# Performance work log

Measured on AMD Instinct MI355X. Metric: run time of the kernel, lower is better.

## Reference

```python
import jax, jax.numpy as jnp
import numpy as np

N_LAYERS, HEADS, D_IN, D_OUT, T, D, DFF = 4, 8, 16, 3, 1024, 512, 2048
D_HEAD = D // HEADS


def sinusoidal_pos_enc(t, d):
    # Faithful to the source: base = pos / 10000**(emb_idx/d); sin on even cols, cos on odd cols
    pos = jnp.arange(t, dtype=jnp.float32)[:, None]
    emb = jnp.arange(d, dtype=jnp.float32)[None, :]
    base = pos / jnp.power(10000.0, emb / d)
    even = (jnp.arange(d) % 2 == 0)[None, :]
    return jnp.where(even, jnp.sin(base), jnp.cos(base))  # (t, d)


def layer_norm(x, g, b, eps=1e-5):
    m = x.mean(-1, keepdims=True)
    v = ((x - m) ** 2).mean(-1, keepdims=True)
    return (x - m) / jnp.sqrt(v + eps) * g + b


def setup_inputs() -> dict:
    key = jax.random.key(0)
    ks = iter(jax.random.split(key, 24))
    s = 0.02
    inp = {}
    inp['x'] = jax.random.normal(next(ks), (16, T, D_IN), dtype=jnp.float32)
    inp['pad_mask'] = jax.random.randint(next(ks), (16, T), 0, 2, dtype=jnp.int32)
    inp['enc_W'] = jax.random.normal(next(ks), (D_IN, D), dtype=jnp.float32) * s
    inp['enc_b'] = jnp.zeros((D,), jnp.float32)
    for name in ['Wq', 'Wk', 'Wv', 'Wo']:
        inp[name] = jax.random.normal(next(ks), (N_LAYERS, D, D), dtype=jnp.float32) * s
    inp['ff_W1'] = jax.random.normal(next(ks), (N_LAYERS, D, DFF), dtype=jnp.float32) * s
    inp['ff_b1'] = jnp.zeros((N_LAYERS, DFF), jnp.float32)
    inp['ff_W2'] = jax.random.normal(next(ks), (N_LAYERS, DFF, D), dtype=jnp.float32) * s
    inp['ff_b2'] = jnp.zeros((N_LAYERS, D), jnp.float32)
    inp['ln1_g'] = jnp.ones((N_LAYERS, D), jnp.float32)
    inp['ln1_b'] = jnp.zeros((N_LAYERS, D), jnp.float32)
    inp['ln2_g'] = jnp.ones((N_LAYERS, D), jnp.float32)
    inp['ln2_b'] = jnp.zeros((N_LAYERS, D), jnp.float32)
    inp['out_W'] = jax.random.normal(next(ks), (D * T, D_OUT), dtype=jnp.float32) * s
    inp['out_b'] = jnp.zeros((D_OUT,), jnp.float32)
    return inp


def reference(x, enc_W, enc_b, Wq, Wk, Wv, Wo, ff_W1, ff_b1, ff_W2, ff_b2,
              ln1_g, ln1_b, ln2_g, ln2_b, out_W, out_b, pad_mask):
    n, t = x.shape[0], x.shape[1]
    # InputEncoding (linear) scaled by sqrt(d_model)
    h = (x @ enc_W + enc_b) * jnp.sqrt(jnp.float32(D))
    # Sinusoidal positional encoding, zeroed at masked (pad_mask==0) timesteps
    pe = sinusoidal_pos_enc(t, D)[None]  # (1, t, d)
    pe = jnp.where(pad_mask[..., None] == 0, 0.0, pe)  # (n, t, d)
    h = h + pe
    mask4 = (pad_mask[..., None, None] == 0)  # (n, t, 1, 1)
    for i in range(N_LAYERS):
        # --- MultiHeadAttention (faithful to source's transpose quirk) ---
        Qh = (h @ Wq[i]).reshape(n, t, HEADS, D_HEAD).swapaxes(2, 3)  # (n,t,dh,H)
        Kh = (h @ Wk[i]).reshape(n, t, HEADS, D_HEAD)                 # (n,t,H,dh)
        Vh = (h @ Wv[i]).reshape(n, t, HEADS, D_HEAD).swapaxes(2, 3)  # (n,t,dh,H)
        # energy: per-timestep (dh x dh), scaled by d_head**1/2 == d_head/2 (source precedence)
        energy = jnp.matmul(Qh, Kh) / (D_HEAD / 2.0)                  # (n,t,dh,dh)
        energy = jnp.where(mask4, -1e20, energy)
        attn = jax.nn.softmax(energy, axis=-1)
        head = jnp.matmul(attn, Vh)                                   # (n,t,dh,H)
        out = head.reshape(n, t, D) @ Wo[i]
        # residual + layer norm
        h = layer_norm(out + h, ln1_g[i], ln1_b[i])
        # --- FFN (relu) ---
        ff = jax.nn.relu(h @ ff_W1[i] + ff_b1[i]) @ ff_W2[i] + ff_b2[i]
        h = layer_norm(ff + h, ln2_g[i], ln2_b[i])
    # mode='train': flatten and project
    return h.reshape(n, -1) @ out_W + out_b  # (n, d_output)
```

## Files before the change

### kernel.cpp

```cpp
#include <hip/hip_runtime.h>
#include <cmath>

#define NB 16
#define TSEQ 1024
#define DIN 16
#define DM 512
#define DFFN 2048
#define NLAYERS 4
#define DOUTN 3
#define ROWS (NB*TSEQ)

typedef unsigned short u16;
typedef short bf16x8 __attribute__((ext_vector_type(8)));
typedef u16   u16x4  __attribute__((ext_vector_type(4)));
typedef float f32x4  __attribute__((ext_vector_type(4)));

__device__ __forceinline__ float b2f(u16 v) { return __uint_as_float((unsigned)v << 16); }
__device__ __forceinline__ u16 f2b(float f) {
    unsigned u = __float_as_uint(f);
    return (u16)((u + 0x7FFFu + ((u >> 16) & 1u)) >> 16);
}

#define GLL(gp, lp) __builtin_amdgcn_global_load_lds( \
    (const __attribute__((address_space(1))) unsigned int*)(gp), \
    (__attribute__((address_space(3))) unsigned int*)(lp), 16, 0, 0)

__global__ __launch_bounds__(256) void transpose_cast(
    const float* __restrict__ in, u16* __restrict__ out,
    int K, int N, size_t in_lstride, size_t out_lstride)
{
    in  += (size_t)blockIdx.z * in_lstride;
    out += (size_t)blockIdx.z * out_lstride;
    __shared__ float t[32][33];
    int bk = blockIdx.x * 32, bn = blockIdx.y * 32;
    int x = threadIdx.x & 31, y = threadIdx.x >> 5;
    #pragma unroll
    for (int i = 0; i < 32; i += 8)
        t[y + i][x] = in[(size_t)(bk + y + i) * N + bn + x];
    __syncthreads();
    #pragma unroll
    for (int i = 0; i < 32; i += 8)
        out[(size_t)(bn + y + i) * K + bk + x] = f2b(t[x][y + i]);
}

__global__ __launch_bounds__(128) void encode_kernel(
    const float* __restrict__ x, const int* __restrict__ pad,
    const float* __restrict__ W, const float* __restrict__ b,
    u16* __restrict__ h)
{
    int row = blockIdx.x;
    int t   = row & (TSEQ - 1);
    int c   = threadIdx.x * 4;
    float acc[4];
    #pragma unroll
    for (int j = 0; j < 4; ++j) acc[j] = b[c + j];
    const float* xr = x + (size_t)row * DIN;
    #pragma unroll
    for (int k = 0; k < DIN; ++k) {
        float xv = xr[k];
        const float* wr = W + (size_t)k * DM + c;
        #pragma unroll
        for (int j = 0; j < 4; ++j) acc[j] += xv * wr[j];
    }
    const float s = 22.62741699796952f;
    bool has_pe = (pad[row] != 0);
    u16x4 o;
    #pragma unroll
    for (int j = 0; j < 4; ++j) {
        acc[j] *= s;
        if (has_pe) {
            int d = c + j;
            float base = (float)t * powf(10000.0f, -(float)d * (1.0f/512.0f));
            acc[j] += ((d & 1) == 0) ? sinf(base) : cosf(base);
        }
        o[j] = f2b(acc[j]);
    }
    *(u16x4*)&h[(size_t)row * DM + c] = o;
}

template<int BIAS, int RELU>
__global__ __launch_bounds__(256) void gemm_bf16(
    const u16* __restrict__ A, const u16* __restrict__ Bt,
    const float* __restrict__ bias, u16* __restrict__ C,
    int M, int N, int K)
{
    __shared__ u16 As[128 * 64];
    __shared__ u16 Bs[128 * 64];
    const int tid  = threadIdx.x;
    const int lane = tid & 63;
    const int wid  = tid >> 6;
    const int wr   = wid >> 1, wc = wid & 1;
    const int bm   = blockIdx.x * 128;
    const int bn   = blockIdx.y * 128;

    const int srow8 = lane >> 3;
    const int sslot = lane & 7;
    const int scol  = ((sslot ^ srow8) * 8);
    const u16* Ag = A  + (size_t)(bm + wid * 32 + srow8) * K + scol;
    const u16* Bg = Bt + (size_t)(bn + wid * 32 + srow8) * K + scol;
    u16* Al = As + wid * 2048;
    u16* Bl = Bs + wid * 2048;

    f32x4 acc[4][4];
    #pragma unroll
    for (int m = 0; m < 4; ++m)
        #pragma unroll
        for (int n = 0; n < 4; ++n)
            acc[m][n] = (f32x4){0.f, 0.f, 0.f, 0.f};

    const int fr  = lane & 15;
    const int grp = lane >> 4;

    for (int k0 = 0; k0 < K; k0 += 64) {
        #pragma unroll
        for (int i = 0; i < 4; ++i) {
            GLL(Ag + (size_t)(i * 8) * K + k0, Al + i * 512);
            GLL(Bg + (size_t)(i * 8) * K + k0, Bl + i * 512);
        }
        __syncthreads();
        bf16x8 a[4][2];
        #pragma unroll
        for (int m = 0; m < 4; ++m) {
            int row = wr * 64 + m * 16 + fr;
            #pragma unroll
            for (int ks = 0; ks < 2; ++ks) {
                int slot = (ks * 4 + grp) ^ (row & 7);
                a[m][ks] = *(const bf16x8*)(As + row * 64 + slot * 8);
            }
        }
        #pragma unroll
        for (int n = 0; n < 4; ++n) {
            bf16x8 b[2];
            int row = wc * 64 + n * 16 + fr;
            #pragma unroll
            for (int ks = 0; ks < 2; ++ks) {
                int slot = (ks * 4 + grp) ^ (row & 7);
                b[ks] = *(const bf16x8*)(Bs + row * 64 + slot * 8);
            }
            #pragma unroll
            for (int m = 0; m < 4; ++m) {
                acc[m][n] = __builtin_amdgcn_mfma_f32_16x16x32_bf16(a[m][0], b[0], acc[m][n], 0, 0, 0);
                acc[m][n] = __builtin_amdgcn_mfma_f32_16x16x32_bf16(a[m][1], b[1], acc[m][n], 0, 0, 0);
            }
        }
        __syncthreads();
    }

    float bb[4] = {0.f, 0.f, 0.f, 0.f};
    if (BIAS) {
        #pragma unroll
        for (int n = 0; n < 4; ++n) bb[n] = bias[bn + wc * 64 + n * 16 + fr];
    }
    #pragma unroll
    for (int m = 0; m < 4; ++m) {
        #pragma unroll
        for (int n = 0; n < 4; ++n) {
            int col = bn + wc * 64 + n * 16 + fr;
            #pragma unroll
            for (int j = 0; j < 4; ++j) {
                int row = bm + wr * 64 + m * 16 + ((lane >> 4) << 2) + j;
                float v = acc[m][n][j];
                if (BIAS) v += bb[n];
                if (RELU) v = fmaxf(v, 0.f);
                C[(size_t)row * N + col] = f2b(v);
            }
        }
    }
}

__global__ __launch_bounds__(256) void attn_mfma(
    const u16* __restrict__ QKV, const int* __restrict__ pad,
    u16* __restrict__ O)
{
    constexpr int WLDS = 6208;
    __shared__ u16 sh[4 * WLDS];
    const int wid  = threadIdx.x >> 6;
    const int lane = threadIdx.x & 63;
    const int site = blockIdx.x * 4 + wid;
    u16* Ql = sh + wid * WLDS;
    u16* Kl = Ql + 512;
    u16* Vl = Ql + 1024;
    u16* P  = Ql + 1600;
    u16* Ol = Ql + 5696;

    const u16* base = QKV + (size_t)site * 1536;
    *(bf16x8*)(Ql + lane * 8) = *(const bf16x8*)(base + lane * 8);
    *(bf16x8*)(Kl + lane * 8) = *(const bf16x8*)(base + 512 + lane * 8);
    {
        bf16x8 v = *(const bf16x8*)(base + 1024 + lane * 8);
        *(bf16x8*)(Vl + (lane >> 3) * 72 + (lane & 7) * 8) = v;
    }

    const int fr  = lane & 15;
    const int grp = lane >> 4;
    const bool masked = (pad[site] == 0);
    const bf16x8 zb = {0,0,0,0,0,0,0,0};
    const f32x4  zf = {0.f,0.f,0.f,0.f};

    if (masked) {
        const u16 c = f2b(1.0f / 64.0f);
        bf16x8 cv = {(short)c,(short)c,(short)c,(short)c,(short)c,(short)c,(short)c,(short)c};
        #pragma unroll
        for (int i = 0; i < 8; ++i)
            *(bf16x8*)(P + i * 512 + lane * 8) = cv;
    } else {
        bf16x8 aq[4], bk[4];
        #pragma unroll
        for (int m = 0; m < 4; ++m) { aq[m] = zb; bk[m] = zb; }
        if (grp == 0) {
            #pragma unroll
            for (int m = 0; m < 4; ++m)
                #pragma unroll
                for (int j = 0; j < 8; ++j) {
                    aq[m][j] = (short)Ql[j * 64 + m * 16 + fr];
                    bk[m][j] = (short)Kl[j * 64 + m * 16 + fr];
                }
        }
        #pragma unroll
        for (int m = 0; m < 4; ++m) {
            f32x4 ev[4];
            #pragma unroll
            for (int n = 0; n < 4; ++n)
                ev[n] = __builtin_amdgcn_mfma_f32_16x16x32_bf16(aq[m], bk[n], zf, 0, 0, 0);
            #pragma unroll
            for (int j = 0; j < 4; ++j) {
                float v = fmaxf(fmaxf(ev[0][j], ev[1][j]), fmaxf(ev[2][j], ev[3][j]));
                v = fmaxf(v, __shfl_xor(v, 1));
                v = fmaxf(v, __shfl_xor(v, 2));
                v = fmaxf(v, __shfl_xor(v, 4));
                v = fmaxf(v, __shfl_xor(v, 8));
                float p0 = __expf((ev[0][j] - v) * 0.03125f);
                float p1 = __expf((ev[1][j] - v) * 0.03125f);
                float p2 = __expf((ev[2][j] - v) * 0.03125f);
                float p3 = __expf((ev[3][j] - v) * 0.03125f);
                float s = p0 + p1 + p2 + p3;
                s += __shfl_xor(s, 1);
                s += __shfl_xor(s, 2);
                s += __shfl_xor(s, 4);
                s += __shfl_xor(s, 8);
                float inv = 1.0f / s;
                int row = m * 16 + grp * 4 + j;
                int sw  = (row & 7) << 3;
                P[(row * 64 +  0 + fr) ^ sw] = f2b(p0 * inv);
                P[(row * 64 + 16 + fr) ^ sw] = f2b(p1 * inv);
                P[(row * 64 + 32 + fr) ^ sw] = f2b(p2 * inv);
                P[(row * 64 + 48 + fr) ^ sw] = f2b(p3 * inv);
            }
        }
    }

    bf16x8 bv[2];
    #pragma unroll
    for (int ks = 0; ks < 2; ++ks) {
        int kb = ks * 32 + grp * 8;
        bv[ks] = (fr < 8) ? *(const bf16x8*)(Vl + fr * 72 + kb) : zb;
    }
    f32x4 pv[4];
    #pragma unroll
    for (int m = 0; m < 4; ++m) pv[m] = zf;
    #pragma unroll
    for (int m = 0; m < 4; ++m) {
        #pragma unroll
        for (int ks = 0; ks < 2; ++ks) {
            int row = m * 16 + fr;
            int off = (row * 64 + ks * 32 + grp * 8) ^ ((row & 7) << 3);
            bf16x8 ap = *(const bf16x8*)(P + off);
            pv[m] = __builtin_amdgcn_mfma_f32_16x16x32_bf16(ap, bv[ks], pv[m], 0, 0, 0);
        }
    }
    #pragma unroll
    for (int m = 0; m < 4; ++m)
        #pragma unroll
        for (int j = 0; j < 4; ++j) {
            int row = m * 16 + grp * 4 + j;
            if (fr < 8) Ol[row * 8 + fr] = f2b(pv[m][j]);
        }
    bf16x8 o = *(const bf16x8*)(Ol + lane * 8);
    *(bf16x8*)(O + (size_t)site * DM + lane * 8) = o;
}

__global__ __launch_bounds__(256) void add_ln_kernel(
    const u16* __restrict__ A, u16* __restrict__ H,
    const float* __restrict__ g, const float* __restrict__ b)
{
    int row  = blockIdx.x * 4 + (threadIdx.x >> 6);
    int lane = threadIdx.x & 63;
    const u16* a = A + (size_t)row * DM + lane * 8;
    u16* h = H + (size_t)row * DM + lane * 8;
    bf16x8 av = *(const bf16x8*)a;
    bf16x8 hv = *(const bf16x8*)h;
    float v[8];
    float s = 0.f;
    #pragma unroll
    for (int j = 0; j < 8; ++j) { v[j] = b2f((u16)av[j]) + b2f((u16)hv[j]); s += v[j]; }
    #pragma unroll
    for (int off = 32; off > 0; off >>= 1) s += __shfl_xor(s, off, 64);
    float mean = s * (1.0f / 512.0f);
    float var = 0.f;
    #pragma unroll
    for (int j = 0; j < 8; ++j) { float d = v[j] - mean; var += d * d; }
    #pragma unroll
    for (int off = 32; off > 0; off >>= 1) var += __shfl_xor(var, off, 64);
    float rstd = rsqrtf(var * (1.0f / 512.0f) + 1e-5f);
    bf16x8 ov;
    #pragma unroll
    for (int j = 0; j < 8; ++j) {
        int d = lane * 8 + j;
        ov[j] = (short)f2b((v[j] - mean) * rstd * g[d] + b[d]);
    }
    *(bf16x8*)h = ov;
}

__global__ __launch_bounds__(256) void out_stage1(
    const u16* __restrict__ h, const float* __restrict__ W,
    float* __restrict__ partial)
{
    int b = blockIdx.x, s = blockIdx.y;
    int tid = threadIdx.x;
    const u16* hb = h + (size_t)b * (TSEQ * DM) + (size_t)s * 8192;
    const float* Wb = W + (size_t)s * 8192 * 3;
    float a0 = 0.f, a1 = 0.f, a2 = 0.f;
    #pragma unroll 4
    for (int it = 0; it < 32; ++it) {
        int i = it * 256 + tid;
        float hv = b2f(hb[i]);
        a0 += hv * Wb[i * 3 + 0];
        a1 += hv * Wb[i * 3 + 1];
        a2 += hv * Wb[i * 3 + 2];
    }
    __shared__ float red[3][256];
    red[0][tid] = a0; red[1][tid] = a1; red[2][tid] = a2;
    __syncthreads();
    for (int off = 128; off > 0; off >>= 1) {
        if (tid < off) {
            red[0][tid] += red[0][tid + off];
            red[1][tid] += red[1][tid + off];
            red[2][tid] += red[2][tid + off];
        }
        __syncthreads();
    }
    if (tid == 0) {
        partial[(b * 64 + s) * 3 + 0] = red[0][0];
        partial[(b * 64 + s) * 3 + 1] = red[1][0];
        partial[(b * 64 + s) * 3 + 2] = red[2][0];
    }
}

__global__ __launch_bounds__(64) void out_stage2(
    const float* __restrict__ partial, const float* __restrict__ ob,
    float* __restrict__ out)
{
    int t = threadIdx.x;
    if (t < NB * DOUTN) {
        int b = t / 3, o = t % 3;
        float s = ob[o];
        for (int k = 0; k < 64; ++k) s += partial[(b * 64 + k) * 3 + o];
        out[t] = s;
    }
}

extern "C" void kernel_launch(void* const* d_in, const int* in_sizes, int n_in,
                              void* d_out, int out_size, void* d_ws, size_t ws_size,
                              hipStream_t stream)
{
    const float* x    = (const float*)d_in[0];
    const int*   pad  = (const int*)  d_in[1];
    const float* encW = (const float*)d_in[2];
    const float* encB = (const float*)d_in[3];
    const float* Wq   = (const float*)d_in[4];
    const float* Wk   = (const float*)d_in[5];
    const float* Wv   = (const float*)d_in[6];
    const float* Wo   = (const float*)d_in[7];
    const float* fW1  = (const float*)d_in[8];
    const float* fb1  = (const float*)d_in[9];
    const float* fW2  = (const float*)d_in[10];
    const float* fb2  = (const float*)d_in[11];
    const float* l1g  = (const float*)d_in[12];
    const float* l1b  = (const float*)d_in[13];
    const float* l2g  = (const float*)d_in[14];
    const float* l2b  = (const float*)d_in[15];
    const float* outW = (const float*)d_in[16];
    const float* outB = (const float*)d_in[17];
    float* out = (float*)d_out;

    const size_t WL  = 3145728;
    const size_t BUF = (size_t)ROWS * DM;
    const size_t need = (4 * WL + 6 * BUF) * sizeof(u16);
    if (ws_size < need) return;
    u16* wt = (u16*)d_ws;
    u16* h  = wt + 4 * WL;
    u16* b0 = h  + BUF;
    u16* b3 = b0 + 3 * BUF;
    u16* b4 = b3 + BUF;

    transpose_cast<<<dim3(16,16,4), 256, 0, stream>>>(Wq,  wt + 0,       512,  512,  (size_t)512*512,  WL);
    transpose_cast<<<dim3(16,16,4), 256, 0, stream>>>(Wk,  wt + 262144,  512,  512,  (size_t)512*512,  WL);
    transpose_cast<<<dim3(16,16,4), 256, 0, stream>>>(Wv,  wt + 524288,  512,  512,  (size_t)512*512,  WL);
    transpose_cast<<<dim3(16,16,4), 256, 0, stream>>>(Wo,  wt + 786432,  512,  512,  (size_t)512*512,  WL);
    transpose_cast<<<dim3(16,64,4), 256, 0, stream>>>(fW1, wt + 1048576, 512,  2048, (size_t)512*2048, WL);
    transpose_cast<<<dim3(64,16,4), 256, 0, stream>>>(fW2, wt + 2097152, 2048, 512,  (size_t)2048*512, WL);

    encode_kernel<<<ROWS, 128, 0, stream>>>(x, pad, encW, encB, h);

    for (int l = 0; l < NLAYERS; ++l) {
        u16* wl = wt + (size_t)l * WL;
        gemm_bf16<0,0><<<dim3(128,12), 256, 0, stream>>>(h, wl, nullptr, b0, ROWS, 1536, DM);
        attn_mfma<<<ROWS/4, 256, 0, stream>>>(b0, pad, b3);
        gemm_bf16<0,0><<<dim3(128,4), 256, 0, stream>>>(b3, wl + 786432, nullptr, b4, ROWS, DM, DM);
        add_ln_kernel<<<ROWS/4, 256, 0, stream>>>(b4, h, l1g + l*DM, l1b + l*DM);
        gemm_bf16<1,1><<<dim3(128,16), 256, 0, stream>>>(h, wl + 1048576, fb1 + (size_t)l*DFFN, b0, ROWS, DFFN, DM);
        gemm_bf16<1,0><<<dim3(128,4),  256, 0, stream>>>(b0, wl + 2097152, fb2 + (size_t)l*DM, b4, ROWS, DM, DFFN);
        add_ln_kernel<<<ROWS/4, 256, 0, stream>>>(b4, h, l2g + l*DM, l2b + l*DM);
    }

    out_stage1<<<dim3(NB, 64), 256, 0, stream>>>(h, outW, (float*)b0);
    out_stage2<<<1, 64, 0, stream>>>((float*)b0, outB, out);
}
```

Baseline: 852.8 us.

## Permute Q/K columns in QKV GEMM epilogue and shrink attention LDS footprint

The QKV GEMM epilogue now writes the Q and K columns in a transposed head-interleaved order, so the attention kernel can load its MFMA operands directly from global memory instead of staging Q, K and V through LDS with scalar gathers. Masked sites skip the softmax and the P·V MFMA and instead write the per-head mean of V directly. The attention P matrix is stored in two halves through a smaller swizzled LDS buffer, with the second half kept in registers until the first half has been consumed. This cuts per-wave LDS from about 12 KB to 5 KB, which raises occupancy, at the cost of scattered 2-byte stores in the QKV epilogue.

```diff
diff --git a/kernel.cpp b/kernel.cpp
--- a/kernel.cpp
+++ b/kernel.cpp
@@ -11,6 +11,7 @@
 #define ROWS (NB*TSEQ)
 
 typedef unsigned short u16;
+typedef unsigned int   u32;
 typedef short bf16x8 __attribute__((ext_vector_type(8)));
 typedef u16   u16x4  __attribute__((ext_vector_type(4)));
 typedef float f32x4  __attribute__((ext_vector_type(4)));
@@ -78,7 +79,7 @@
     *(u16x4*)&h[(size_t)row * DM + c] = o;
 }
 
-template<int BIAS, int RELU>
+template<int BIAS, int RELU, int QKPERM>
 __global__ __launch_bounds__(256) void gemm_bf16(
     const u16* __restrict__ A, const u16* __restrict__ Bt,
     const float* __restrict__ bias, u16* __restrict__ C,
@@ -156,13 +157,18 @@
         #pragma unroll
         for (int n = 0; n < 4; ++n) {
             int col = bn + wc * 64 + n * 16 + fr;
+            int colw = col;
+            if (QKPERM) {
+                if (col < 1024)
+                    colw = (col & 512) | (((col & 63) << 3) | ((col >> 6) & 7));
+            }
             #pragma unroll
             for (int j = 0; j < 4; ++j) {
                 int row = bm + wr * 64 + m * 16 + ((lane >> 4) << 2) + j;
                 float v = acc[m][n][j];
                 if (BIAS) v += bb[n];
                 if (RELU) v = fmaxf(v, 0.f);
-                C[(size_t)row * N + col] = f2b(v);
+                C[(size_t)row * N + colw] = f2b(v);
             }
         }
     }
@@ -172,102 +178,105 @@
     const u16* __restrict__ QKV, const int* __restrict__ pad,
     u16* __restrict__ O)
 {
-    constexpr int WLDS = 6208;
+    constexpr int WLDS = 2560;
     __shared__ u16 sh[4 * WLDS];
     const int wid  = threadIdx.x >> 6;
     const int lane = threadIdx.x & 63;
     const int site = blockIdx.x * 4 + wid;
-    u16* Ql = sh + wid * WLDS;
-    u16* Kl = Ql + 512;
-    u16* Vl = Ql + 1024;
-    u16* P  = Ql + 1600;
-    u16* Ol = Ql + 5696;
+    u16* P2 = sh + wid * WLDS;
+    u16* Ol = P2 + 2048;
 
     const u16* base = QKV + (size_t)site * 1536;
-    *(bf16x8*)(Ql + lane * 8) = *(const bf16x8*)(base + lane * 8);
-    *(bf16x8*)(Kl + lane * 8) = *(const bf16x8*)(base + 512 + lane * 8);
-    {
-        bf16x8 v = *(const bf16x8*)(base + 1024 + lane * 8);
-        *(bf16x8*)(Vl + (lane >> 3) * 72 + (lane & 7) * 8) = v;
-    }
-
     const int fr  = lane & 15;
     const int grp = lane >> 4;
-    const bool masked = (pad[site] == 0);
     const bf16x8 zb = {0,0,0,0,0,0,0,0};
     const f32x4  zf = {0.f,0.f,0.f,0.f};
 
-    if (masked) {
-        const u16 c = f2b(1.0f / 64.0f);
-        bf16x8 cv = {(short)c,(short)c,(short)c,(short)c,(short)c,(short)c,(short)c,(short)c};
-        #pragma unroll
-        for (int i = 0; i < 8; ++i)
-            *(bf16x8*)(P + i * 512 + lane * 8) = cv;
-    } else {
-        bf16x8 aq[4], bk[4];
-        #pragma unroll
-        for (int m = 0; m < 4; ++m) { aq[m] = zb; bk[m] = zb; }
-        if (grp == 0) {
-            #pragma unroll
-            for (int m = 0; m < 4; ++m)
-                #pragma unroll
-                for (int j = 0; j < 8; ++j) {
-                    aq[m][j] = (short)Ql[j * 64 + m * 16 + fr];
-                    bk[m][j] = (short)Kl[j * 64 + m * 16 + fr];
-                }
-        }
-        #pragma unroll
-        for (int m = 0; m < 4; ++m) {
-            f32x4 ev[4];
-            #pragma unroll
-            for (int n = 0; n < 4; ++n)
-                ev[n] = __builtin_amdgcn_mfma_f32_16x16x32_bf16(aq[m], bk[n], zf, 0, 0, 0);
-            #pragma unroll
-            for (int j = 0; j < 4; ++j) {
-                float v = fmaxf(fmaxf(ev[0][j], ev[1][j]), fmaxf(ev[2][j], ev[3][j]));
-                v = fmaxf(v, __shfl_xor(v, 1));
-                v = fmaxf(v, __shfl_xor(v, 2));
-                v = fmaxf(v, __shfl_xor(v, 4));
-                v = fmaxf(v, __shfl_xor(v, 8));
-                float p0 = __expf((ev[0][j] - v) * 0.03125f);
-                float p1 = __expf((ev[1][j] - v) * 0.03125f);
-                float p2 = __expf((ev[2][j] - v) * 0.03125f);
-                float p3 = __expf((ev[3][j] - v) * 0.03125f);
-                float s = p0 + p1 + p2 + p3;
-                s += __shfl_xor(s, 1);
-                s += __shfl_xor(s, 2);
-                s += __shfl_xor(s, 4);
-                s += __shfl_xor(s, 8);
-                float inv = 1.0f / s;
-                int row = m * 16 + grp * 4 + j;
-                int sw  = (row & 7) << 3;
-                P[(row * 64 +  0 + fr) ^ sw] = f2b(p0 * inv);
-                P[(row * 64 + 16 + fr) ^ sw] = f2b(p1 * inv);
-                P[(row * 64 + 32 + fr) ^ sw] = f2b(p2 * inv);
-                P[(row * 64 + 48 + fr) ^ sw] = f2b(p3 * inv);
-            }
-        }
-    }
-
+    if (pad[site] == 0) {
+        bf16x8 vv = *(const bf16x8*)(base + 1024 + lane * 8);
+        float s = 0.f;
+        #pragma unroll
+        for (int j = 0; j < 8; ++j) s += b2f((u16)vv[j]);
+        s += __shfl_xor(s, 1); s += __shfl_xor(s, 2); s += __shfl_xor(s, 4);
+        s *= (1.0f / 64.0f);
+        bf16x8 ov;
+        #pragma unroll
+        for (int h2 = 0; h2 < 8; ++h2) ov[h2] = (short)f2b(__shfl(s, h2 * 8));
+        *(bf16x8*)(O + (size_t)site * DM + lane * 8) = ov;
+        return;
+    }
+
+    bf16x8 bk[4];
+    #pragma unroll
+    for (int n = 0; n < 4; ++n)
+        bk[n] = (grp == 0) ? *(const bf16x8*)(base + 512 + (n * 16 + fr) * 8) : zb;
     bf16x8 bv[2];
     #pragma unroll
-    for (int ks = 0; ks < 2; ++ks) {
-        int kb = ks * 32 + grp * 8;
-        bv[ks] = (fr < 8) ? *(const bf16x8*)(Vl + fr * 72 + kb) : zb;
-    }
+    for (int ks = 0; ks < 2; ++ks)
+        bv[ks] = (fr < 8) ? *(const bf16x8*)(base + 1024 + fr * 64 + ks * 32 + grp * 8) : zb;
+
+    u32 p23[16];
+    #pragma unroll
+    for (int m = 0; m < 4; ++m) {
+        bf16x8 aq = (grp == 0) ? *(const bf16x8*)(base + (m * 16 + fr) * 8) : zb;
+        f32x4 ev[4];
+        #pragma unroll
+        for (int n = 0; n < 4; ++n)
+            ev[n] = __builtin_amdgcn_mfma_f32_16x16x32_bf16(aq, bk[n], zf, 0, 0, 0);
+        #pragma unroll
+        for (int j = 0; j < 4; ++j) {
+            float v = fmaxf(fmaxf(ev[0][j], ev[1][j]), fmaxf(ev[2][j], ev[3][j]));
+            v = fmaxf(v, __shfl_xor(v, 1));
+            v = fmaxf(v, __shfl_xor(v, 2));
+            v = fmaxf(v, __shfl_xor(v, 4));
+            v = fmaxf(v, __shfl_xor(v, 8));
+            float p0 = __expf((ev[0][j] - v) * 0.03125f);
+            float p1 = __expf((ev[1][j] - v) * 0.03125f);
+            float p2 = __expf((ev[2][j] - v) * 0.03125f);
+            float p3 = __expf((ev[3][j] - v) * 0.03125f);
+            float s = p0 + p1 + p2 + p3;
+            s += __shfl_xor(s, 1);
+            s += __shfl_xor(s, 2);
+            s += __shfl_xor(s, 4);
+            s += __shfl_xor(s, 8);
+            float inv = 1.0f / s;
+            int r  = m * 16 + grp * 4 + j;
+            int sw = j ^ grp;
+            P2[r * 32 + (((fr >> 3) ^ sw) * 8) + (fr & 7)]       = f2b(p0 * inv);
+            P2[r * 32 + (((2 + (fr >> 3)) ^ sw) * 8) + (fr & 7)] = f2b(p1 * inv);
+            p23[m * 4 + j] = (u32)f2b(p2 * inv) | ((u32)f2b(p3 * inv) << 16);
+        }
+    }
+
     f32x4 pv[4];
     #pragma unroll
-    for (int m = 0; m < 4; ++m) pv[m] = zf;
-    #pragma unroll
     for (int m = 0; m < 4; ++m) {
-        #pragma unroll
-        for (int ks = 0; ks < 2; ++ks) {
-            int row = m * 16 + fr;
-            int off = (row * 64 + ks * 32 + grp * 8) ^ ((row & 7) << 3);
-            bf16x8 ap = *(const bf16x8*)(P + off);
-            pv[m] = __builtin_amdgcn_mfma_f32_16x16x32_bf16(ap, bv[ks], pv[m], 0, 0, 0);
-        }
-    }
+        int row = m * 16 + fr;
+        int slot = grp ^ (fr & 3) ^ (fr >> 2);
+        bf16x8 ap = *(const bf16x8*)(P2 + row * 32 + slot * 8);
+        pv[m] = __builtin_amdgcn_mfma_f32_16x16x32_bf16(ap, bv[0], zf, 0, 0, 0);
+    }
+    asm volatile("s_waitcnt lgkmcnt(0)" ::: "memory");
+    __builtin_amdgcn_sched_barrier(0);
+
+    #pragma unroll
+    for (int m = 0; m < 4; ++m)
+        #pragma unroll
+        for (int j = 0; j < 4; ++j) {
+            int r  = m * 16 + grp * 4 + j;
+            int sw = j ^ grp;
+            u32 pk = p23[m * 4 + j];
+            P2[r * 32 + (((fr >> 3) ^ sw) * 8) + (fr & 7)]       = (u16)(pk & 0xFFFF);
+            P2[r * 32 + (((2 + (fr >> 3)) ^ sw) * 8) + (fr & 7)] = (u16)(pk >> 16);
+        }
+    #pragma unroll
+    for (int m = 0; m < 4; ++m) {
+        int row = m * 16 + fr;
+        int slot = grp ^ (fr & 3) ^ (fr >> 2);
+        bf16x8 ap = *(const bf16x8*)(P2 + row * 32 + slot * 8);
+        pv[m] = __builtin_amdgcn_mfma_f32_16x16x32_bf16(ap, bv[1], pv[m], 0, 0, 0);
+    }
+
     #pragma unroll
     for (int m = 0; m < 4; ++m)
         #pragma unroll
@@ -404,12 +413,12 @@
 
     for (int l = 0; l < NLAYERS; ++l) {
         u16* wl = wt + (size_t)l * WL;
-        gemm_bf16<0,0><<<dim3(128,12), 256, 0, stream>>>(h, wl, nullptr, b0, ROWS, 1536, DM);
+        gemm_bf16<0,0,1><<<dim3(128,12), 256, 0, stream>>>(h, wl, nullptr, b0, ROWS, 1536, DM);
         attn_mfma<<<ROWS/4, 256, 0, stream>>>(b0, pad, b3);
-        gemm_bf16<0,0><<<dim3(128,4), 256, 0, stream>>>(b3, wl + 786432, nullptr, b4, ROWS, DM, DM);
+        gemm_bf16<0,0,0><<<dim3(128,4), 256, 0, stream>>>(b3, wl + 786432, nullptr, b4, ROWS, DM, DM);
         add_ln_kernel<<<ROWS/4, 256, 0, stream>>>(b4, h, l1g + l*DM, l1b + l*DM);
-        gemm_bf16<1,1><<<dim3(128,16), 256, 0, stream>>>(h, wl + 1048576, fb1 + (size_t)l*DFFN, b0, ROWS, DFFN, DM);
-        gemm_bf16<1,0><<<dim3(128,4),  256, 0, stream>>>(b0, wl + 2097152, fb2 + (size_t)l*DM, b4, ROWS, DM, DFFN);
+        gemm_bf16<1,1,0><<<dim3(128,16), 256, 0, stream>>>(h, wl + 1048576, fb1 + (size_t)l*DFFN, b0, ROWS, DFFN, DM);
+        gemm_bf16<1,0,0><<<dim3(128,4),  256, 0, stream>>>(b0, wl + 2097152, fb2 + (size_t)l*DM, b4, ROWS, DM, DFFN);
         add_ln_kernel<<<ROWS/4, 256, 0, stream>>>(b4, h, l2g + l*DM, l2b + l*DM);
     }
 
```

Result: slower. 919.0 us (+7.8%).
